# Kernel tuning notes

Measured on AMD Instinct MI355X. Metric: run time of the kernel, lower is better.

## Reference

```python
import jax, jax.numpy as jnp
import numpy as np
from jax import lax

EPS = 1e-5  # BatchNorm eps (torch default)

def _up2_bilinear_ac(x):
    # bilinear upsample x2, align_corners=True; x: [B,C,H,W]
    B, C, H, W = x.shape
    def axis_interp(n_in, n_out):
        pos = jnp.arange(n_out, dtype=jnp.float32) * ((n_in - 1) / (n_out - 1))
        i0 = jnp.floor(pos).astype(jnp.int32)
        i1 = jnp.minimum(i0 + 1, n_in - 1)
        w = (pos - i0.astype(jnp.float32)).astype(x.dtype)
        return i0, i1, w
    i0, i1, wh = axis_interp(H, 2 * H)
    x = x[:, :, i0, :] * (1.0 - wh)[None, None, :, None] + x[:, :, i1, :] * wh[None, None, :, None]
    j0, j1, ww = axis_interp(W, 2 * W)
    x = x[:, :, :, j0] * (1.0 - ww) + x[:, :, :, j1] * ww
    return x

def setup_inputs() -> dict:
    key = jax.random.key(0)
    ks = jax.random.split(key, 8)
    B, Cin, Cout, H, W = 8, 64, 32, 128, 128
    att, K = 16, 2  # attention_channel = max(int(64*0.0625),16)=16; kernel_num=2
    n = lambda k, s, sc: jax.random.normal(k, s, jnp.float32) * sc
    return {
        'x': n(ks[0], (B, Cin, H, W), 1.0),
        'fc_w': n(ks[1], (att, Cin), 0.1),
        'bn_a_gamma': jnp.ones((att,), jnp.float32), 'bn_a_beta': jnp.zeros((att,), jnp.float32),
        'bn_a_mean': jnp.zeros((att,), jnp.float32), 'bn_a_var': jnp.ones((att,), jnp.float32),
        'ch_w': n(ks[2], (Cin, att), 0.1), 'ch_b': jnp.zeros((Cin,), jnp.float32),
        'fil_w': n(ks[3], (Cout, att), 0.1), 'fil_b': jnp.zeros((Cout,), jnp.float32),
        'sp_w': n(ks[4], (9, att), 0.1), 'sp_b': jnp.zeros((9,), jnp.float32),
        'k_w': n(ks[5], (K, att), 0.1), 'k_b': jnp.zeros((K,), jnp.float32),
        'weight': n(ks[6], (K, Cout, Cin, 3, 3), 0.05),
        'bn_gamma': jnp.ones((Cout,), jnp.float32), 'bn_beta': jnp.zeros((Cout,), jnp.float32),
        'bn_mean': jnp.zeros((Cout,), jnp.float32), 'bn_var': jnp.ones((Cout,), jnp.float32),
    }

def reference(x, fc_w, bn_a_gamma, bn_a_beta, bn_a_mean, bn_a_var,
              ch_w, ch_b, fil_w, fil_b, sp_w, sp_b, k_w, k_b,
              weight, bn_gamma, bn_beta, bn_mean, bn_var):
    x = _up2_bilinear_ac(x)
    B, Cin, H, W = x.shape
    K, Cout = weight.shape[0], weight.shape[1]
    # --- ODConv attention branch (on GAP features) ---
    g = x.mean(axis=(2, 3))                                    # [B,Cin]
    h = g @ fc_w.T                                             # [B,att]
    h = (h - bn_a_mean) / jnp.sqrt(bn_a_var + EPS) * bn_a_gamma + bn_a_beta
    h = jax.nn.relu(h)
    ch_att = jax.nn.sigmoid(h @ ch_w.T + ch_b)                 # [B,Cin]
    fil_att = jax.nn.sigmoid(h @ fil_w.T + fil_b)              # [B,Cout]
    sp_att = jax.nn.sigmoid(h @ sp_w.T + sp_b).reshape(B, 1, 1, 1, 3, 3)
    k_att = jax.nn.softmax(h @ k_w.T + k_b, axis=1).reshape(B, K, 1, 1, 1, 1)
    # per-sample aggregated filters: [B,Cout,Cin,3,3]
    agg_w = jnp.sum(k_att * sp_att * weight[None], axis=1)
    # --- dynamic conv (per-sample filter), channel-attended input ---
    x = x * ch_att[:, :, None, None]
    def conv1(xi, wi):
        return lax.conv_general_dilated(xi[None], wi, (1, 1), [(1, 1), (1, 1)],
                                        dimension_numbers=('NCHW', 'OIHW', 'NCHW'))[0]
    y = jax.vmap(conv1)(x, agg_w)                              # [B,Cout,H,W]
    y = y * fil_att[:, :, None, None]
    # --- BatchNorm2d (inference) + GELU (exact erf) ---
    y = (y - bn_mean[:, None, None]) / jnp.sqrt(bn_var[:, None, None] + EPS)
    y = y * bn_gamma[:, None, None] + bn_beta[:, None, None]
    return jax.nn.gelu(y, approximate=False)
```

## Files before the change

kernel.cpp:

```cpp
#include <hip/hip_runtime.h>
#include <hip/hip_bf16.h>

#define EPSBN 1e-5f

typedef short short8 __attribute__((ext_vector_type(8)));
typedef float f32x16 __attribute__((ext_vector_type(16)));

static __device__ __forceinline__ unsigned short f2u(float f){
  __hip_bfloat16 h = __float2bfloat16(f);
  union { __hip_bfloat16 h; unsigned short u; } c; c.h = h; return c.u;
}

#define WS_G     2048
#define WS_S     7168
#define WS_T     8192
#define WS_AGGB  16384
#define WS_XUP   327680

__global__ __launch_bounds__(256) void k_up(const float* __restrict__ x,
                                            unsigned int* __restrict__ xup32,
                                            float* __restrict__ g)
{
  __shared__ float xin[16*798];
  __shared__ float w[128];
  int tid = threadIdx.x;
  int bi  = blockIdx.x;
  int strip = bi & 31, h16 = (bi >> 5) & 3, b = bi >> 7;
  int r0 = strip * 8;
  int i0b = (int)((float)r0 * (127.0f/255.0f));

  if (tid < 128){
    int i = tid;
    float s = 0.f;
    int rstart = max(0, (int)floorf((float)(i-1)*(255.0f/127.0f)));
    #pragma unroll
    for (int k = 0; k < 8; ++k){
      int r = rstart + k;
      if (r <= 255){
        float pos = (float)r * (127.0f/255.0f);
        int i0 = (int)pos; float fr = pos - (float)i0; int i1 = min(i0+1,127);
        if (i0 == i) s += 1.0f - fr;
        if (i1 == i) s += fr;
      }
    }
    w[i] = s;
  }
  for (int e = tid; e < 12288; e += 256){
    int ir = e >> 11, rem = e & 2047, ci = rem >> 7, j = rem & 127;
    int row = min(i0b + ir, 127);
    xin[ci*798 + ir*133 + j] = x[(((size_t)(b*64 + h16*16 + ci)) << 14) + (row << 7) + j];
  }
  __syncthreads();

  {
    int ci_l = tid >> 4, kk = tid & 15;
    float s = 0.f;
    const float* base = &xin[ci_l*798];
    #pragma unroll
    for (int row = 0; row < 4; ++row){
      int grow = 4*strip + row;
      int ir = grow - i0b;
      const float* rp = base + ir*133 + kk*8;
      float ss = 0.f;
      #pragma unroll
      for (int j = 0; j < 8; ++j) ss += rp[j]*w[kk*8+j];
      s += w[grow]*ss;
    }
    s += __shfl_down(s, 8, 16);
    s += __shfl_down(s, 4, 16);
    s += __shfl_down(s, 2, 16);
    s += __shfl_down(s, 1, 16);
    if (kk == 0) atomicAdd(&g[b*64 + h16*16 + ci_l], s*(1.0f/65536.0f));
  }

  int ci2 = tid & 7, cbase = tid >> 3;
  int j0t[8], j1t[8]; float wwt[8];
  #pragma unroll
  for (int jj = 0; jj < 8; ++jj){
    int c = cbase + 32*jj;
    float pos = (float)c * (127.0f/255.0f);
    int j0 = (int)pos;
    j0t[jj] = j0; j1t[jj] = min(j0+1,127); wwt[jj] = pos - (float)j0;
  }
  const float* base0 = &xin[(ci2*2+0)*798];
  const float* base1 = &xin[(ci2*2+1)*798];
  size_t plane32 = ((size_t)(b*4 + h16)) << 19;

  for (int rr = 0; rr < 8; ++rr){
    int r = r0 + rr;
    float posr = (float)r * (127.0f/255.0f);
    int i0 = (int)posr; float wh = posr - (float)i0;
    int ir0 = (i0 - i0b)*133, ir1 = (min(i0+1,127) - i0b)*133;
    #pragma unroll
    for (int jj = 0; jj < 8; ++jj){
      int c = cbase + 32*jj;
      int j0 = j0t[jj], j1 = j1t[jj]; float ww = wwt[jj];
      float v00 = base0[ir0+j0], v01 = base0[ir0+j1];
      float v10 = base0[ir1+j0], v11 = base0[ir1+j1];
      float a0 = v00 + (v01-v00)*ww;
      float a1 = v10 + (v11-v10)*ww;
      float r0v = a0 + (a1-a0)*wh;
      float u00 = base1[ir0+j0], u01 = base1[ir0+j1];
      float u10 = base1[ir1+j0], u11 = base1[ir1+j1];
      float b0 = u00 + (u01-u00)*ww;
      float b1 = u10 + (u11-u10)*ww;
      float r1v = b0 + (b1-b0)*wh;
      unsigned pack = (unsigned)f2u(r0v) | (((unsigned)f2u(r1v)) << 16);
      xup32[plane32 + (size_t)(r*256 + c)*8 + ci2] = pack;
    }
  }
}

__global__ __launch_bounds__(256) void k_aggw(const float* __restrict__ g,
                      const float* __restrict__ fc_w,
                      const float* __restrict__ bga, const float* __restrict__ bba,
                      const float* __restrict__ bma, const float* __restrict__ bva,
                      const float* __restrict__ ch_w, const float* __restrict__ ch_b,
                      const float* __restrict__ fil_w, const float* __restrict__ fil_b,
                      const float* __restrict__ sp_w, const float* __restrict__ sp_b,
                      const float* __restrict__ k_w, const float* __restrict__ k_b,
                      const float* __restrict__ bn_g, const float* __restrict__ bn_b,
                      const float* __restrict__ bn_m, const float* __restrict__ bn_v,
                      const float* __restrict__ weight,
                      unsigned short* __restrict__ aggb,
                      float* __restrict__ sS, float* __restrict__ tT)
{
  __shared__ float h[8][16];
  int tid = threadIdx.x;
  if (tid < 128){
    int b = tid >> 4, a = tid & 15;
    float acc = 0.f;
    for (int c = 0; c < 64; ++c) acc += g[b*64+c] * fc_w[a*64+c];
    float v = (acc - bma[a]) * rsqrtf(bva[a] + EPSBN) * bga[a] + bba[a];
    h[b][a] = fmaxf(v, 0.f);
  }
  __syncthreads();

  int idx = blockIdx.x*256 + tid;
  int ci_l = idx & 31;
  int o    = (idx >> 5) & 31;
  int s    = (idx >> 10) % 9;
  int t2   = (idx >> 10) / 9;
  int cc   = t2 & 1, b = t2 >> 1;
  int ci   = cc*32 + ci_l;

  const float* hb = h[b];
  float zc = ch_b[ci], zs = sp_b[s];
  float z0 = k_b[0],  z1 = k_b[1];
  #pragma unroll
  for (int a = 0; a < 16; ++a){
    float hv = hb[a];
    zc += hv*ch_w[ci*16+a];
    zs += hv*sp_w[s*16+a];
    z0 += hv*k_w[a];
    z1 += hv*k_w[16+a];
  }
  float chv = 1.f/(1.f+expf(-zc));
  float spv = 1.f/(1.f+expf(-zs));
  float m = fmaxf(z0,z1);
  float e0 = expf(z0-m), e1 = expf(z1-m), inv = 1.f/(e0+e1);
  float ka0 = e0*inv, ka1 = e1*inv;
  float w0 = weight[(o*64+ci)*9+s];
  float w1 = weight[((32+o)*64+ci)*9+s];
  aggb[idx] = f2u(chv*spv*(ka0*w0 + ka1*w1));

  if (blockIdx.x == 0){
    int bb = tid >> 5, oo = tid & 31;
    float z = fil_b[oo];
    #pragma unroll
    for (int a = 0; a < 16; ++a) z += h[bb][a]*fil_w[oo*16+a];
    float f = 1.f/(1.f+expf(-z));
    float invs = rsqrtf(bn_v[oo] + EPSBN);
    sS[tid] = f * bn_g[oo] * invs;
    if (bb == 0) tT[oo] = bn_b[oo] - bn_m[oo]*bn_g[oo]*invs;
  }
}

#define XT_STRIDE 40

static __device__ __forceinline__ void xdesc(int e, int p0, int q0,
                                             int& ldso, int& pmo, bool& v){
  int rr = e / 72; int rem = e - rr*72;
  int qq = rem >> 2; int k2 = (rem >> 1) & 1; int kqe = rem & 1;
  int gr = p0 - 1 + rr, gq = q0 - 1 + qq;
  v    = ((unsigned)gr < 256u) && ((unsigned)gq < 256u);
  ldso = (rr*18+qq)*XT_STRIDE + k2*16 + kqe*8;
  pmo  = (k2 << 20) + (gr*256+gq)*16 + kqe*8;
}

__global__ __launch_bounds__(256) void k_conv(const unsigned short* __restrict__ xup,
                                              const unsigned short* __restrict__ aggb,
                                              const float* __restrict__ sS,
                                              const float* __restrict__ tT,
                                              float* __restrict__ out)
{
  __shared__ unsigned short xt[18*18*XT_STRIDE];
  __shared__ float sSs[32], tTs[32];

  int tid = threadIdx.x;
  int bi  = blockIdx.x;
  int b   = bi >> 8, t = bi & 255;
  int p0  = (t >> 4) * 16, q0 = (t & 15) * 16;
  int lane = tid & 63, wv = tid >> 6;
  if (tid < 32){ sSs[tid] = sS[b*32+tid]; tTs[tid] = tT[tid]; }

  f32x16 acc[2];
  #pragma unroll
  for (int i = 0; i < 16; ++i){ acc[0][i] = 0.f; acc[1][i] = 0.f; }

  int n  = lane & 31;
  int kq = lane >> 5;
  int lr0 = 2*(2*wv + 0) + (n >> 4);
  int lr1 = 2*(2*wv + 1) + (n >> 4);
  int qb  = n & 15;

  const unsigned short* xb0 = xup + (((size_t)(b*4 + 0)) << 20);
  const unsigned short* xb1 = xup + (((size_t)(b*4 + 2)) << 20);
  const short8 zero8 = {0,0,0,0,0,0,0,0};

  #pragma unroll
  for (int k = 0; k < 6; ++k){
    int e = tid + (k << 8); if (e >= 1296) e -= 1296;
    int ldso, pmo; bool v;
    xdesc(e, p0, q0, ldso, pmo, v);
    short8 vv = zero8;
    if (v) vv = *(const short8*)&xb0[pmo];
    *(short8*)&xt[ldso] = vv;
  }
  short8 pre[6];
  #pragma unroll
  for (int k = 0; k < 6; ++k){
    int e = tid + (k << 8); if (e >= 1296) e -= 1296;
    int ldso, pmo; bool v;
    xdesc(e, p0, q0, ldso, pmo, v);
    pre[k] = zero8;
    if (v) pre[k] = *(const short8*)&xb1[pmo];
  }
  __syncthreads();

  auto kloop = [&](const unsigned short* ab){
    short8 a0 = *(const short8*)&ab[0];
    short8 a1 = *(const short8*)&ab[16];
    #pragma unroll
    for (int s = 0; s < 9; ++s){
      int sn = (s < 8) ? s+1 : 8;
      short8 na0 = *(const short8*)&ab[sn*1024];
      short8 na1 = *(const short8*)&ab[sn*1024+16];
      const int ky = s/3, kx = s%3;
      {
        const unsigned short* xrow = &xt[((lr0+ky)*18 + qb+kx)*XT_STRIDE + kq*8];
        short8 bv0 = *(const short8*)&xrow[0];
        short8 bv1 = *(const short8*)&xrow[16];
        acc[0] = __builtin_amdgcn_mfma_f32_32x32x16_bf16(a0, bv0, acc[0], 0, 0, 0);
        acc[0] = __builtin_amdgcn_mfma_f32_32x32x16_bf16(a1, bv1, acc[0], 0, 0, 0);
      }
      {
        const unsigned short* xrow = &xt[((lr1+ky)*18 + qb+kx)*XT_STRIDE + kq*8];
        short8 bv0 = *(const short8*)&xrow[0];
        short8 bv1 = *(const short8*)&xrow[16];
        acc[1] = __builtin_amdgcn_mfma_f32_32x32x16_bf16(a0, bv0, acc[1], 0, 0, 0);
        acc[1] = __builtin_amdgcn_mfma_f32_32x32x16_bf16(a1, bv1, acc[1], 0, 0, 0);
      }
      a0 = na0; a1 = na1;
    }
  };

  kloop(aggb + (size_t)(b*2+0)*9216 + n*32 + kq*8);
  __syncthreads();
  #pragma unroll
  for (int k = 0; k < 6; ++k){
    int e = tid + (k << 8); if (e >= 1296) e -= 1296;
    int ldso, pmo; bool v;
    xdesc(e, p0, q0, ldso, pmo, v);
    *(short8*)&xt[ldso] = pre[k];
  }
  __syncthreads();
  kloop(aggb + (size_t)(b*2+1)*9216 + n*32 + kq*8);

  #pragma unroll
  for (int tt = 0; tt < 2; ++tt){
    int lr = (tt == 0) ? lr0 : lr1;
    int p = p0 + lr, q = q0 + qb;
    #pragma unroll
    for (int r = 0; r < 16; ++r){
      int o = (r & 3) + 8*(r >> 2) + 4*kq;
      float valv = acc[tt][r]*sSs[o] + tTs[o];
      float gl  = 0.5f*valv*(1.f + erff(valv*0.70710678118f));
      out[(((size_t)(b*32+o)) << 16) + (p << 8) + q] = gl;
    }
  }
}

extern "C" void kernel_launch(void* const* d_in, const int* in_sizes, int n_in,
                              void* d_out, int out_size, void* d_ws, size_t ws_size,
                              hipStream_t stream)
{
  const float* x     = (const float*)d_in[0];
  const float* fc_w  = (const float*)d_in[1];
  const float* bga   = (const float*)d_in[2];
  const float* bba   = (const float*)d_in[3];
  const float* bma   = (const float*)d_in[4];
  const float* bva   = (const float*)d_in[5];
  const float* ch_w  = (const float*)d_in[6];
  const float* ch_b  = (const float*)d_in[7];
  const float* fil_w = (const float*)d_in[8];
  const float* fil_b = (const float*)d_in[9];
  const float* sp_w  = (const float*)d_in[10];
  const float* sp_b  = (const float*)d_in[11];
  const float* k_w   = (const float*)d_in[12];
  const float* k_b   = (const float*)d_in[13];
  const float* weight= (const float*)d_in[14];
  const float* bn_g  = (const float*)d_in[15];
  const float* bn_b  = (const float*)d_in[16];
  const float* bn_m  = (const float*)d_in[17];
  const float* bn_v  = (const float*)d_in[18];

  char* ws = (char*)d_ws;
  float* g   = (float*)(ws + WS_G);
  float* sS  = (float*)(ws + WS_S);
  float* tT  = (float*)(ws + WS_T);
  unsigned short* aggb = (unsigned short*)(ws + WS_AGGB);
  unsigned short* xup  = (unsigned short*)(ws + WS_XUP);
  float* out = (float*)d_out;

  hipMemsetAsync(g, 0, 512*sizeof(float), stream);
  hipLaunchKernelGGL(k_up,   dim3(1024), dim3(256), 0, stream, x, (unsigned int*)xup, g);
  hipLaunchKernelGGL(k_aggw, dim3(576),  dim3(256), 0, stream, g, fc_w, bga, bba, bma, bva,
                     ch_w, ch_b, fil_w, fil_b, sp_w, sp_b, k_w, k_b,
                     bn_g, bn_b, bn_m, bn_v, weight, aggb, sS, tT);
  hipLaunchKernelGGL(k_conv, dim3(2048), dim3(256), 0, stream, xup, aggb, sS, tT, out);
}
```

Before: 191.0 us.

## Drop LDS staging in conv; read MFMA operands straight from global with interior fast path

```diff
diff --git a/kernel.cpp b/kernel.cpp
--- a/kernel.cpp
+++ b/kernel.cpp
@@ -176,16 +176,41 @@
   }
 }
 
-#define XT_STRIDE 40
-
-static __device__ __forceinline__ void xdesc(int e, int p0, int q0,
-                                             int& ldso, int& pmo, bool& v){
-  int rr = e / 72; int rem = e - rr*72;
-  int qq = rem >> 2; int k2 = (rem >> 1) & 1; int kqe = rem & 1;
-  int gr = p0 - 1 + rr, gq = q0 - 1 + qq;
-  v    = ((unsigned)gr < 256u) && ((unsigned)gq < 256u);
-  ldso = (rr*18+qq)*XT_STRIDE + k2*16 + kqe*8;
-  pmo  = (k2 << 20) + (gr*256+gq)*16 + kqe*8;
+template<bool CHK>
+static __device__ __forceinline__ void conv_body(
+    const unsigned short* __restrict__ xup,
+    const unsigned short* __restrict__ aggb,
+    int b, int p0, int q0, int wv, int n, int kq,
+    f32x16* acc)
+{
+  const short8 zero8 = {0,0,0,0,0,0,0,0};
+  const int rp = n >> 4, qb = n & 15;
+  #pragma unroll
+  for (int cc = 0; cc < 2; ++cc){
+    const unsigned short* ap  = aggb + (size_t)(b*2+cc)*9216 + n*32 + kq*8;
+    const unsigned short* pl0 = xup + (((size_t)(b*4 + cc*2)) << 20) + kq*8;
+    const unsigned short* pl1 = pl0 + (1u << 20);
+    #pragma unroll
+    for (int s = 0; s < 9; ++s){
+      short8 a0 = *(const short8*)&ap[s*1024];
+      short8 a1 = *(const short8*)&ap[s*1024 + 16];
+      const int ky = s/3, kx = s%3;
+      #pragma unroll
+      for (int tt = 0; tt < 2; ++tt){
+        int gr = p0 - 1 + 4*wv + 2*tt + rp + ky;
+        int gq = q0 - 1 + qb + kx;
+        short8 b0 = zero8, b1 = zero8;
+        bool v = !CHK || (((unsigned)gr < 256u) && ((unsigned)gq < 256u));
+        if (v){
+          int off = (gr*256 + gq)*16;
+          b0 = *(const short8*)&pl0[off];
+          b1 = *(const short8*)&pl1[off];
+        }
+        acc[tt] = __builtin_amdgcn_mfma_f32_32x32x16_bf16(a0, b0, acc[tt], 0, 0, 0);
+        acc[tt] = __builtin_amdgcn_mfma_f32_32x32x16_bf16(a1, b1, acc[tt], 0, 0, 0);
+      }
+    }
+  }
 }
 
 __global__ __launch_bounds__(256) void k_conv(const unsigned short* __restrict__ xup,
@@ -194,97 +219,32 @@
                                               const float* __restrict__ tT,
                                               float* __restrict__ out)
 {
-  __shared__ unsigned short xt[18*18*XT_STRIDE];
-  __shared__ float sSs[32], tTs[32];
-
   int tid = threadIdx.x;
   int bi  = blockIdx.x;
   int b   = bi >> 8, t = bi & 255;
   int p0  = (t >> 4) * 16, q0 = (t & 15) * 16;
   int lane = tid & 63, wv = tid >> 6;
-  if (tid < 32){ sSs[tid] = sS[b*32+tid]; tTs[tid] = tT[tid]; }
-
-  f32x16 acc[2];
-  #pragma unroll
-  for (int i = 0; i < 16; ++i){ acc[0][i] = 0.f; acc[1][i] = 0.f; }
-
   int n  = lane & 31;
   int kq = lane >> 5;
-  int lr0 = 2*(2*wv + 0) + (n >> 4);
-  int lr1 = 2*(2*wv + 1) + (n >> 4);
-  int qb  = n & 15;
-
-  const unsigned short* xb0 = xup + (((size_t)(b*4 + 0)) << 20);
-  const unsigned short* xb1 = xup + (((size_t)(b*4 + 2)) << 20);
-  const short8 zero8 = {0,0,0,0,0,0,0,0};
-
-  #pragma unroll
-  for (int k = 0; k < 6; ++k){
-    int e = tid + (k << 8); if (e >= 1296) e -= 1296;
-    int ldso, pmo; bool v;
-    xdesc(e, p0, q0, ldso, pmo, v);
-    short8 vv = zero8;
-    if (v) vv = *(const short8*)&xb0[pmo];
-    *(short8*)&xt[ldso] = vv;
-  }
-  short8 pre[6];
-  #pragma unroll
-  for (int k = 0; k < 6; ++k){
-    int e = tid + (k << 8); if (e >= 1296) e -= 1296;
-    int ldso, pmo; bool v;
-    xdesc(e, p0, q0, ldso, pmo, v);
-    pre[k] = zero8;
-    if (v) pre[k] = *(const short8*)&xb1[pmo];
-  }
-  __syncthreads();
-
-  auto kloop = [&](const unsigned short* ab){
-    short8 a0 = *(const short8*)&ab[0];
-    short8 a1 = *(const short8*)&ab[16];
-    #pragma unroll
-    for (int s = 0; s < 9; ++s){
-      int sn = (s < 8) ? s+1 : 8;
-      short8 na0 = *(const short8*)&ab[sn*1024];
-      short8 na1 = *(const short8*)&ab[sn*1024+16];
-      const int ky = s/3, kx = s%3;
-      {
-        const unsigned short* xrow = &xt[((lr0+ky)*18 + qb+kx)*XT_STRIDE + kq*8];
-        short8 bv0 = *(const short8*)&xrow[0];
-        short8 bv1 = *(const short8*)&xrow[16];
-        acc[0] = __builtin_amdgcn_mfma_f32_32x32x16_bf16(a0, bv0, acc[0], 0, 0, 0);
-        acc[0] = __builtin_amdgcn_mfma_f32_32x32x16_bf16(a1, bv1, acc[0], 0, 0, 0);
-      }
-      {
-        const unsigned short* xrow = &xt[((lr1+ky)*18 + qb+kx)*XT_STRIDE + kq*8];
-        short8 bv0 = *(const short8*)&xrow[0];
-        short8 bv1 = *(const short8*)&xrow[16];
-        acc[1] = __builtin_amdgcn_mfma_f32_32x32x16_bf16(a0, bv0, acc[1], 0, 0, 0);
-        acc[1] = __builtin_amdgcn_mfma_f32_32x32x16_bf16(a1, bv1, acc[1], 0, 0, 0);
-      }
-      a0 = na0; a1 = na1;
-    }
-  };
-
-  kloop(aggb + (size_t)(b*2+0)*9216 + n*32 + kq*8);
-  __syncthreads();
-  #pragma unroll
-  for (int k = 0; k < 6; ++k){
-    int e = tid + (k << 8); if (e >= 1296) e -= 1296;
-    int ldso, pmo; bool v;
-    xdesc(e, p0, q0, ldso, pmo, v);
-    *(short8*)&xt[ldso] = pre[k];
-  }
-  __syncthreads();
-  kloop(aggb + (size_t)(b*2+1)*9216 + n*32 + kq*8);
-
+
+  f32x16 acc[2];
+  #pragma unroll
+  for (int i = 0; i < 16; ++i){ acc[0][i] = 0.f; acc[1][i] = 0.f; }
+
+  bool interior = (p0 != 0) && (p0 != 240) && (q0 != 0) && (q0 != 240);
+  if (interior) conv_body<false>(xup, aggb, b, p0, q0, wv, n, kq, acc);
+  else          conv_body<true >(xup, aggb, b, p0, q0, wv, n, kq, acc);
+
+  int rp = n >> 4, qb = n & 15;
   #pragma unroll
   for (int tt = 0; tt < 2; ++tt){
-    int lr = (tt == 0) ? lr0 : lr1;
+    int lr = 4*wv + 2*tt + rp;
     int p = p0 + lr, q = q0 + qb;
     #pragma unroll
     for (int r = 0; r < 16; ++r){
       int o = (r & 3) + 8*(r >> 2) + 4*kq;
-      float valv = acc[tt][r]*sSs[o] + tTs[o];
+      float sv = sS[b*32+o], tv = tT[o];
+      float valv = acc[tt][r]*sv + tv;
       float gl  = 0.5f*valv*(1.f + erff(valv*0.70710678118f));
       out[(((size_t)(b*32+o)) << 16) + (p << 8) + q] = gl;
     }
```

After: 198.6 us. 4.0% more time.
